# Optimization experiments

Hardware: AMD Instinct MI355X
Metric: run time of the kernel (lower is better)

## Reference

```python
import jax, jax.numpy as jnp
import numpy as np

V, G, D = 512, 4, 64


def setup_inputs() -> dict:
    key = jax.random.key(0)
    k1, k2, k3 = jax.random.split(key, 3)
    GE = jax.random.randint(k1, (V, G, 1), 0, 3, dtype=jnp.int64)
    # nn.Linear(3, D): weight [D,3], bias [D]; store transposed as [3,D]
    W = jax.random.normal(k2, (3, D), dtype=jnp.float32)
    b = jax.random.normal(k3, (D,), dtype=jnp.float32)
    return {"GE": GE, "W": W, "b": b}


def reference(GE, W, b):
    # one-hot per (vertex, graph): [V, G, 3]
    oh = jax.nn.one_hot(GE[..., 0] % 3, 3, dtype=W.dtype)
    # Linear(3, D) on the one-hot (commutes with the repeat): [V, G, D]
    emb = jnp.einsum('vgk,kd->vgd', oh, W) + b
    # repeat along a new vertex axis -> [V, G, V, D]
    return jnp.broadcast_to(emb[:, :, None, :], (V, G, V, D))
```

## Files before the change

### kernel.cpp

```cpp
#include <hip/hip_runtime.h>
#include <hip/hip_bf16.h>


#define V 512
#define G 4
#define D 64
#define D4 (D / 4)

typedef float fx4 __attribute__((ext_vector_type(4)));

__global__ __launch_bounds__(256) void gembed_kernel(
    const int* __restrict__ GE,
    const float* __restrict__ W,
    const float* __restrict__ b,
    float* __restrict__ out)
{
    const int bid = blockIdx.x;
    const int tid = threadIdx.x;
    const int d4  = tid & (D4 - 1);
    const int u0  = tid >> 4;

    int e = GE[bid];
    e = ((e % 3) + 3) % 3;

    const fx4* __restrict__ W4 = (const fx4*)W;
    const fx4* __restrict__ b4 = (const fx4*)b;

    fx4 val = W4[e * D4 + d4] + b4[d4];

    fx4* __restrict__ out4 = (fx4*)out + (size_t)bid * (V * D4)
                                       + (size_t)u0 * D4 + d4;

    #pragma unroll
    for (int k = 0; k < 32; ++k) {
        __builtin_nontemporal_store(val, out4);
        out4 += 16 * D4;
    }
}

extern "C" void kernel_launch(void* const* d_in, const int* in_sizes, int n_in,
                              void* d_out, int out_size, void* d_ws, size_t ws_size,
                              hipStream_t stream) {
    const int*   GE = (const int*)d_in[0];
    const float* W  = (const float*)d_in[1];
    const float* b  = (const float*)d_in[2];
    float* out = (float*)d_out;

    gembed_kernel<<<V * G, 256, 0, stream>>>(GE, W, b, out);
}
```

Measured before the change: 267.7 us.

## Switch to grid-stride flat store loop with per-element GE lookup

Replaces the one-block-per-(vertex,graph) layout with a fixed grid of 2048 blocks that walks the whole flattened output in a grid-stride loop. Each thread precomputes all three embedding rows and, for every stored vector, reloads GE to pick one. Nontemporal stores become plain stores, and the modulo normalisation of GE is dropped, so values outside 0..2 no longer wrap. This adds a GE load per store and changes the cache policy of the write stream.

```diff
diff --git a/kernel.cpp b/kernel.cpp
--- a/kernel.cpp
+++ b/kernel.cpp
@@ -6,35 +6,39 @@
 #define G 4
 #define D 64
 #define D4 (D / 4)
+#define BIDSHIFT 13
+#define NBLK 2048
+#define NTHR 256
+#define STRIDE (NBLK * NTHR)
+#define TOT4 (V * G * V * D4)
 
 typedef float fx4 __attribute__((ext_vector_type(4)));
 
-__global__ __launch_bounds__(256) void gembed_kernel(
+__global__ __launch_bounds__(NTHR) void gembed_kernel(
     const int* __restrict__ GE,
     const float* __restrict__ W,
     const float* __restrict__ b,
     float* __restrict__ out)
 {
-    const int bid = blockIdx.x;
-    const int tid = threadIdx.x;
-    const int d4  = tid & (D4 - 1);
-    const int u0  = tid >> 4;
-
-    int e = GE[bid];
-    e = ((e % 3) + 3) % 3;
+    const int t = blockIdx.x * NTHR + threadIdx.x;
+    const int d4 = t & (D4 - 1);
 
     const fx4* __restrict__ W4 = (const fx4*)W;
     const fx4* __restrict__ b4 = (const fx4*)b;
 
-    fx4 val = W4[e * D4 + d4] + b4[d4];
+    fx4 bb = b4[d4];
+    fx4 v0 = W4[0 * D4 + d4] + bb;
+    fx4 v1 = W4[1 * D4 + d4] + bb;
+    fx4 v2 = W4[2 * D4 + d4] + bb;
 
-    fx4* __restrict__ out4 = (fx4*)out + (size_t)bid * (V * D4)
-                                       + (size_t)u0 * D4 + d4;
+    fx4* __restrict__ out4 = (fx4*)out;
 
-    #pragma unroll
-    for (int k = 0; k < 32; ++k) {
-        __builtin_nontemporal_store(val, out4);
-        out4 += 16 * D4;
+    #pragma unroll 4
+    for (int idx = t; idx < TOT4; idx += STRIDE) {
+        int bid = idx >> BIDSHIFT;
+        int e = GE[bid];
+        fx4 val = (e == 0) ? v0 : ((e == 1) ? v1 : v2);
+        out4[idx] = val;
     }
 }
 
@@ -46,5 +50,5 @@
     const float* b  = (const float*)d_in[2];
     float* out = (float*)d_out;
 
-    gembed_kernel<<<V * G, 256, 0, stream>>>(GE, W, b, out);
+    gembed_kernel<<<NBLK, NTHR, 0, stream>>>(GE, W, b, out);
 }
```

Result: faster. 261.5 us (-2.3%).
